# Kernel optimization log

Measured on AMD Instinct MI355X. Metric: run time of the kernel, lower is better.

Reference implementation:

```python
import jax, jax.numpy as jnp
import numpy as np

N_USERS = 200000
N_ITEMS = 100000
EMB_DIM = 64
N_LAYERS = 4
E_POS = 2000000
E_NEG = 500000


def _propagate(row, col, user_emb, item_emb, edge_weight, n_users, n_items):
    # LightGCN-style symmetric degree-normalized neighbor aggregation.
    deg_u = jnp.clip(jnp.zeros((n_users,), jnp.float32).at[row].add(1.0), 1.0)
    deg_i = jnp.clip(jnp.zeros((n_items,), jnp.float32).at[col].add(1.0), 1.0)
    norm = jax.lax.rsqrt(deg_u)[row] * jax.lax.rsqrt(deg_i)[col] * edge_weight  # [E]
    # gather -> scale -> scatter_add, both directions
    item_to_user = jnp.zeros_like(user_emb).at[row].add(item_emb[col] * norm[:, None])
    user_to_item = jnp.zeros_like(item_emb).at[col].add(user_emb[row] * norm[:, None])
    return user_emb + item_to_user, item_emb + user_to_item


def setup_inputs() -> dict:
    key = jax.random.key(0)
    k1, k2, k3, k4, k5, k6 = jax.random.split(key, 6)
    # Xavier-normal-ish init: std = sqrt(2/(fan_in+fan_out))
    std_u = np.sqrt(2.0 / (N_USERS + EMB_DIM)).astype(np.float32)
    std_i = np.sqrt(2.0 / (N_ITEMS + EMB_DIM)).astype(np.float32)
    return {
        "edge_index": jax.random.randint(k1, (2, E_POS), 0, N_ITEMS, dtype=jnp.int32),
        "negative_edge_index": jax.random.randint(k2, (2, E_NEG), 0, N_ITEMS, dtype=jnp.int32),
        "edge_weight": jnp.ones((E_POS,), jnp.float32),
        "user_emb_pos_w": jax.random.normal(k3, (N_USERS, EMB_DIM), jnp.float32) * std_u,
        "item_emb_pos_w": jax.random.normal(k4, (N_ITEMS, EMB_DIM), jnp.float32) * std_i,
        "user_emb_neg_w": jax.random.normal(k5, (N_USERS, EMB_DIM), jnp.float32) * std_u,
        "item_emb_neg_w": jax.random.normal(k6, (N_ITEMS, EMB_DIM), jnp.float32) * std_i,
    }


def reference(edge_index, negative_edge_index, edge_weight,
              user_emb_pos_w, item_emb_pos_w, user_emb_neg_w, item_emb_neg_w):
    row, col = edge_index[0], edge_index[1]
    nrow, ncol = negative_edge_index[0], negative_edge_index[1]
    neg_w = jnp.ones_like(nrow, dtype=jnp.float32)

    ue_p, ie_p = user_emb_pos_w, item_emb_pos_w
    ue_n, ie_n = user_emb_neg_w, item_emb_neg_w
    sum_up, sum_ip = ue_p, ie_p
    sum_un, sum_in = ue_n, ie_n
    for _ in range(N_LAYERS):
        ue_p, ie_p = _propagate(row, col, ue_p, ie_p, edge_weight, N_USERS, N_ITEMS)
        sum_up = sum_up + ue_p
        sum_ip = sum_ip + ie_p
    for _ in range(N_LAYERS):
        ue_n, ie_n = _propagate(nrow, ncol, ue_n, ie_n, neg_w, N_USERS, N_ITEMS)
        sum_un = sum_un + ue_n
        sum_in = sum_in + ie_n
    inv = 1.0 / (N_LAYERS + 1)
    return (sum_up * inv, sum_ip * inv, sum_un * inv, sum_in * inv)
```

## Files before the change

kernel.cpp:

```cpp
#include <hip/hip_runtime.h>

#define DIM 64
#define CHUNK 2048


__global__ void hist_kernel(const int* __restrict__ row, const int* __restrict__ col,
                            int* __restrict__ deg_u, int* __restrict__ deg_i, int E) {
    int e = blockIdx.x * blockDim.x + threadIdx.x;
    if (e < E) {
        atomicAdd(&deg_u[row[e]], 1);
        atomicAdd(&deg_i[col[e]], 1);
    }
}

__global__ void fill_rsqrt(const int* __restrict__ deg, float* __restrict__ r, int n) {
    int i = blockIdx.x * blockDim.x + threadIdx.x;
    if (i < n) r[i] = rsqrtf(fmaxf((float)deg[i], 1.0f));
}

__global__ void partial_sums(const int* __restrict__ deg, int* __restrict__ bsum, int n) {
    __shared__ int s[256];
    int t = threadIdx.x;
    int base = blockIdx.x * CHUNK + t * 8;
    int loc = 0;
    for (int k = 0; k < 8; k++) { int j = base + k; if (j < n) loc += deg[j]; }
    s[t] = loc; __syncthreads();
    for (int ofs = 128; ofs > 0; ofs >>= 1) { if (t < ofs) s[t] += s[t + ofs]; __syncthreads(); }
    if (t == 0) bsum[blockIdx.x] = s[0];
}

__global__ void scan_small(int* __restrict__ bsum, int nb) {
    if (threadIdx.x == 0 && blockIdx.x == 0) {
        int acc = 0;
        for (int i = 0; i < nb; i++) { int x = bsum[i]; bsum[i] = acc; acc += x; }
    }
}

__global__ void scan_chunk(const int* __restrict__ deg, int* __restrict__ offs,
                           int* __restrict__ cur, const int* __restrict__ bsum, int n) {
    __shared__ int s[256];
    int t = threadIdx.x;
    int base = blockIdx.x * CHUNK + t * 8;
    int v[8]; int loc = 0;
    for (int k = 0; k < 8; k++) { int j = base + k; v[k] = (j < n) ? deg[j] : 0; loc += v[k]; }
    s[t] = loc; __syncthreads();
    for (int ofs = 1; ofs < 256; ofs <<= 1) {
        int x = (t >= ofs) ? s[t - ofs] : 0;
        __syncthreads();
        s[t] += x;
        __syncthreads();
    }
    int excl = (t == 0) ? 0 : s[t - 1];
    int run = bsum[blockIdx.x] + excl;
    for (int k = 0; k < 8; k++) {
        int j = base + k;
        if (j < n) { offs[j] = run; cur[j] = run; }
        run += v[k];
    }
}

__global__ void scatter_kernel(const int* __restrict__ row, const int* __restrict__ col,
                               const float* __restrict__ w, int has_w,
                               const float* __restrict__ ru, const float* __restrict__ ri,
                               int* __restrict__ cur_u, int* __restrict__ cur_i,
                               int2* __restrict__ adj_u, int2* __restrict__ adj_i, int E) {
    int e = blockIdx.x * blockDim.x + threadIdx.x;
    if (e >= E) return;
    int r = row[e], c = col[e];
    float wv = has_w ? w[e] : 1.0f;
    float nrm = ru[r] * ri[c] * wv;
    int nb = __float_as_int(nrm);
    int pu = atomicAdd(&cur_u[r], 1);
    adj_u[pu] = make_int2(c, nb);
    int pi = atomicAdd(&cur_i[c], 1);
    adj_i[pi] = make_int2(r, nb);
}


__global__ void init2(const float* __restrict__ src, float* __restrict__ cur,
                      float* __restrict__ sum, int n4) {
    int i = blockIdx.x * blockDim.x + threadIdx.x;
    if (i < n4) {
        float4 v = ((const float4*)src)[i];
        ((float4*)cur)[i] = v;
        ((float4*)sum)[i] = v;
    }
}

__global__ void aggregate(const int* __restrict__ offs, const int* __restrict__ endo,
                          const int2* __restrict__ adj,
                          const float* __restrict__ src,
                          const float* __restrict__ self_old,
                          float* __restrict__ self_new,
                          float* __restrict__ sum,
                          float scale, int N) {
    int t = blockIdx.x * blockDim.x + threadIdx.x;
    int v = t >> 4;
    if (v >= N) return;
    int q = (t & 15) * 4;
    size_t rowoff = (size_t)v * DIM + q;
    float4 acc = *(const float4*)(self_old + rowoff);
    int s = offs[v], e = endo[v];
    int i = s;
    for (; i + 1 < e; i += 2) {
        int2 m0 = adj[i];
        int2 m1 = adj[i + 1];
        float n0 = __int_as_float(m0.y);
        float n1 = __int_as_float(m1.y);
        float4 b0 = *(const float4*)(src + (size_t)m0.x * DIM + q);
        float4 b1 = *(const float4*)(src + (size_t)m1.x * DIM + q);
        acc.x += b0.x * n0 + b1.x * n1;
        acc.y += b0.y * n0 + b1.y * n1;
        acc.z += b0.z * n0 + b1.z * n1;
        acc.w += b0.w * n0 + b1.w * n1;
    }
    if (i < e) {
        int2 m0 = adj[i];
        float n0 = __int_as_float(m0.y);
        float4 b0 = *(const float4*)(src + (size_t)m0.x * DIM + q);
        acc.x += b0.x * n0;
        acc.y += b0.y * n0;
        acc.z += b0.z * n0;
        acc.w += b0.w * n0;
    }
    *(float4*)(self_new + rowoff) = acc;
    float4 sm = *(const float4*)(sum + rowoff);
    sm.x = (sm.x + acc.x) * scale;
    sm.y = (sm.y + acc.y) * scale;
    sm.z = (sm.z + acc.z) * scale;
    sm.w = (sm.w + acc.w) * scale;
    *(float4*)(sum + rowoff) = sm;
}


static inline int cdiv(long long a, int b) { return (int)((a + b - 1) / b); }

extern "C" void kernel_launch(void* const* d_in, const int* in_sizes, int n_in,
                              void* d_out, int out_size, void* d_ws, size_t ws_size,
                              hipStream_t stream) {
    const int*   ei  = (const int*)d_in[0];
    const int*   nei = (const int*)d_in[1];
    const float* ew  = (const float*)d_in[2];
    const float* uep = (const float*)d_in[3];
    const float* iep = (const float*)d_in[4];
    const float* uen = (const float*)d_in[5];
    const float* ien = (const float*)d_in[6];
    float* out = (float*)d_out;

    const int E_POS = in_sizes[2];
    const int E_NEG = in_sizes[1] / 2;
    const int NU = in_sizes[3] / DIM;
    const int NI = in_sizes[4] / DIM;
    const int NTOT = (NU + NI) * DIM;

    char* ws = (char*)d_ws;
    size_t off = 0;
    auto alloc = [&](size_t elems4) { void* p = ws + off; off += elems4 * 4; return p; };
    float* u_emb  = (float*)alloc((size_t)NU * DIM);
    float* i_emb0 = (float*)alloc((size_t)NI * DIM);
    float* i_emb1 = (float*)alloc((size_t)NI * DIM);
    int*   offs_u = (int*)alloc(NU);
    int*   offs_i = (int*)alloc(NI);
    int*   cur_u  = (int*)alloc(NU);
    int*   cur_i  = (int*)alloc(NI);
    float* ru     = (float*)alloc(NU);
    float* ri     = (float*)alloc(NI);
    int*   bsum   = (int*)alloc(256);
    int2*  adj_u  = (int2*)alloc((size_t)E_POS * 2);
    int2*  adj_i  = (int2*)alloc((size_t)E_POS * 2);

    const int B = 256;
    const int nb_u = cdiv(NU, CHUNK);
    const int nb_i = cdiv(NI, CHUNK);

    for (int g = 0; g < 2; ++g) {
        const int    E   = g == 0 ? E_POS : E_NEG;
        const int*   row = g == 0 ? ei : nei;
        const int*   col = row + E;
        const float* wv  = g == 0 ? ew : nullptr;
        const float* ue0 = g == 0 ? uep : uen;
        const float* ie0 = g == 0 ? iep : ien;
        float* sum_u = out + (size_t)g * NTOT;
        float* sum_i = sum_u + (size_t)NU * DIM;

        hipMemsetAsync(cur_u, 0, (size_t)(NU + NI) * sizeof(int), stream);
        hist_kernel<<<cdiv(E, B), B, 0, stream>>>(row, col, cur_u, cur_i, E);
        fill_rsqrt<<<cdiv(NU, B), B, 0, stream>>>(cur_u, ru, NU);
        fill_rsqrt<<<cdiv(NI, B), B, 0, stream>>>(cur_i, ri, NI);
        partial_sums<<<nb_u, B, 0, stream>>>(cur_u, bsum, NU);
        scan_small<<<1, 64, 0, stream>>>(bsum, nb_u);
        scan_chunk<<<nb_u, B, 0, stream>>>(cur_u, offs_u, cur_u, bsum, NU);
        partial_sums<<<nb_i, B, 0, stream>>>(cur_i, bsum, NI);
        scan_small<<<1, 64, 0, stream>>>(bsum, nb_i);
        scan_chunk<<<nb_i, B, 0, stream>>>(cur_i, offs_i, cur_i, bsum, NI);
        scatter_kernel<<<cdiv(E, B), B, 0, stream>>>(row, col, wv, g == 0 ? 1 : 0,
                                                     ru, ri, cur_u, cur_i,
                                                     adj_u, adj_i, E);

        init2<<<cdiv(NU * DIM / 4, B), B, 0, stream>>>(ue0, u_emb, sum_u, NU * DIM / 4);
        init2<<<cdiv(NI * DIM / 4, B), B, 0, stream>>>(ie0, i_emb0, sum_i, NI * DIM / 4);

        float* icur = i_emb0;
        float* inew = i_emb1;
        for (int l = 0; l < 4; ++l) {
            float scale = (l == 3) ? 0.2f : 1.0f;
            aggregate<<<cdiv((long long)NI * 16, B), B, 0, stream>>>(
                offs_i, cur_i, adj_i, u_emb, icur, inew, sum_i, scale, NI);
            aggregate<<<cdiv((long long)NU * 16, B), B, 0, stream>>>(
                offs_u, cur_u, adj_u, icur, u_emb, u_emb, sum_u, scale, NU);
            float* t = icur; icur = inew; inew = t;
        }
    }
}
```

Baseline: 1.870 ms.

## Merge user/item CSR into one array and use wave-per-vertex aggregation

Builds a single combined degree/offset/adjacency structure for users and items, which halves the number of histogram-scan launches and replaces the serial single-thread block-sum scan with a parallel block scan. The aggregate kernel now assigns one 64-lane wavefront per vertex, with one float per lane, a wave-uniform vertex index and a 4-way unrolled neighbor loop, instead of 16 lanes per vertex using float4. This is meant to cut launch and serial-scan overhead and to raise memory-level parallelism in the gather. The tradeoff is narrower per-lane loads and more threads per vertex.

```diff
diff --git a/kernel.cpp b/kernel.cpp
--- a/kernel.cpp
+++ b/kernel.cpp
@@ -5,11 +5,11 @@
 
 
 __global__ void hist_kernel(const int* __restrict__ row, const int* __restrict__ col,
-                            int* __restrict__ deg_u, int* __restrict__ deg_i, int E) {
+                            int* __restrict__ deg, int NU, int E) {
     int e = blockIdx.x * blockDim.x + threadIdx.x;
     if (e < E) {
-        atomicAdd(&deg_u[row[e]], 1);
-        atomicAdd(&deg_i[col[e]], 1);
+        atomicAdd(&deg[row[e]], 1);
+        atomicAdd(&deg[NU + col[e]], 1);
     }
 }
 
@@ -29,11 +29,18 @@
     if (t == 0) bsum[blockIdx.x] = s[0];
 }
 
-__global__ void scan_small(int* __restrict__ bsum, int nb) {
-    if (threadIdx.x == 0 && blockIdx.x == 0) {
-        int acc = 0;
-        for (int i = 0; i < nb; i++) { int x = bsum[i]; bsum[i] = acc; acc += x; }
-    }
+__global__ void scan_block(int* __restrict__ bsum, int nb) {
+    __shared__ int s[256];
+    int t = threadIdx.x;
+    int x = (t < nb) ? bsum[t] : 0;
+    s[t] = x; __syncthreads();
+    for (int ofs = 1; ofs < 256; ofs <<= 1) {
+        int y = (t >= ofs) ? s[t - ofs] : 0;
+        __syncthreads();
+        s[t] += y;
+        __syncthreads();
+    }
+    if (t < nb) bsum[t] = s[t] - x;
 }
 
 __global__ void scan_chunk(const int* __restrict__ deg, int* __restrict__ offs,
@@ -61,19 +68,19 @@
 
 __global__ void scatter_kernel(const int* __restrict__ row, const int* __restrict__ col,
                                const float* __restrict__ w, int has_w,
-                               const float* __restrict__ ru, const float* __restrict__ ri,
-                               int* __restrict__ cur_u, int* __restrict__ cur_i,
-                               int2* __restrict__ adj_u, int2* __restrict__ adj_i, int E) {
+                               const float* __restrict__ rs,
+                               int* __restrict__ cur, int2* __restrict__ adj,
+                               int NU, int E) {
     int e = blockIdx.x * blockDim.x + threadIdx.x;
     if (e >= E) return;
     int r = row[e], c = col[e];
     float wv = has_w ? w[e] : 1.0f;
-    float nrm = ru[r] * ri[c] * wv;
+    float nrm = rs[r] * rs[NU + c] * wv;
     int nb = __float_as_int(nrm);
-    int pu = atomicAdd(&cur_u[r], 1);
-    adj_u[pu] = make_int2(c, nb);
-    int pi = atomicAdd(&cur_i[c], 1);
-    adj_i[pi] = make_int2(r, nb);
+    int pu = atomicAdd(&cur[r], 1);
+    adj[pu] = make_int2(c, nb);
+    int pi = atomicAdd(&cur[NU + c], 1);
+    adj[pi] = make_int2(r, nb);
 }
 
 
@@ -94,42 +101,35 @@
                           float* __restrict__ self_new,
                           float* __restrict__ sum,
                           float scale, int N) {
-    int t = blockIdx.x * blockDim.x + threadIdx.x;
-    int v = t >> 4;
+    int v = blockIdx.x * (blockDim.x >> 6) + (threadIdx.x >> 6);
     if (v >= N) return;
-    int q = (t & 15) * 4;
-    size_t rowoff = (size_t)v * DIM + q;
-    float4 acc = *(const float4*)(self_old + rowoff);
+    v = __builtin_amdgcn_readfirstlane(v);
+    int l = threadIdx.x & 63;
+    size_t rowoff = (size_t)v * DIM + l;
+    float acc = self_old[rowoff];
     int s = offs[v], e = endo[v];
     int i = s;
-    for (; i + 1 < e; i += 2) {
+    for (; i + 3 < e; i += 4) {
         int2 m0 = adj[i];
         int2 m1 = adj[i + 1];
-        float n0 = __int_as_float(m0.y);
-        float n1 = __int_as_float(m1.y);
-        float4 b0 = *(const float4*)(src + (size_t)m0.x * DIM + q);
-        float4 b1 = *(const float4*)(src + (size_t)m1.x * DIM + q);
-        acc.x += b0.x * n0 + b1.x * n1;
-        acc.y += b0.y * n0 + b1.y * n1;
-        acc.z += b0.z * n0 + b1.z * n1;
-        acc.w += b0.w * n0 + b1.w * n1;
-    }
-    if (i < e) {
-        int2 m0 = adj[i];
-        float n0 = __int_as_float(m0.y);
-        float4 b0 = *(const float4*)(src + (size_t)m0.x * DIM + q);
-        acc.x += b0.x * n0;
-        acc.y += b0.y * n0;
-        acc.z += b0.z * n0;
-        acc.w += b0.w * n0;
-    }
-    *(float4*)(self_new + rowoff) = acc;
-    float4 sm = *(const float4*)(sum + rowoff);
-    sm.x = (sm.x + acc.x) * scale;
-    sm.y = (sm.y + acc.y) * scale;
-    sm.z = (sm.z + acc.z) * scale;
-    sm.w = (sm.w + acc.w) * scale;
-    *(float4*)(sum + rowoff) = sm;
+        int2 m2 = adj[i + 2];
+        int2 m3 = adj[i + 3];
+        float b0 = src[(size_t)m0.x * DIM + l];
+        float b1 = src[(size_t)m1.x * DIM + l];
+        float b2 = src[(size_t)m2.x * DIM + l];
+        float b3 = src[(size_t)m3.x * DIM + l];
+        acc += b0 * __int_as_float(m0.y);
+        acc += b1 * __int_as_float(m1.y);
+        acc += b2 * __int_as_float(m2.y);
+        acc += b3 * __int_as_float(m3.y);
+    }
+    for (; i < e; i++) {
+        int2 m = adj[i];
+        acc += src[(size_t)m.x * DIM + l] * __int_as_float(m.y);
+    }
+    self_new[rowoff] = acc;
+    float sm = sum[rowoff];
+    sum[rowoff] = (sm + acc) * scale;
 }
 
 
@@ -151,27 +151,23 @@
     const int E_NEG = in_sizes[1] / 2;
     const int NU = in_sizes[3] / DIM;
     const int NI = in_sizes[4] / DIM;
-    const int NTOT = (NU + NI) * DIM;
+    const int NV = NU + NI;
+    const int NTOT = NV * DIM;
 
     char* ws = (char*)d_ws;
     size_t off = 0;
     auto alloc = [&](size_t elems4) { void* p = ws + off; off += elems4 * 4; return p; };
-    float* u_emb  = (float*)alloc((size_t)NU * DIM);
+    float* u_emb = (float*)alloc((size_t)NU * DIM);
     float* i_emb0 = (float*)alloc((size_t)NI * DIM);
     float* i_emb1 = (float*)alloc((size_t)NI * DIM);
-    int*   offs_u = (int*)alloc(NU);
-    int*   offs_i = (int*)alloc(NI);
-    int*   cur_u  = (int*)alloc(NU);
-    int*   cur_i  = (int*)alloc(NI);
-    float* ru     = (float*)alloc(NU);
-    float* ri     = (float*)alloc(NI);
-    int*   bsum   = (int*)alloc(256);
-    int2*  adj_u  = (int2*)alloc((size_t)E_POS * 2);
-    int2*  adj_i  = (int2*)alloc((size_t)E_POS * 2);
+    int*   offs = (int*)alloc(NV);
+    int*   cur  = (int*)alloc(NV);
+    float* rs   = (float*)alloc(NV);
+    int*   bsum = (int*)alloc(256);
+    int2*  adj  = (int2*)alloc((size_t)E_POS * 4);
 
     const int B = 256;
-    const int nb_u = cdiv(NU, CHUNK);
-    const int nb_i = cdiv(NI, CHUNK);
+    const int nb = cdiv(NV, CHUNK);
 
     for (int g = 0; g < 2; ++g) {
         const int    E   = g == 0 ? E_POS : E_NEG;
@@ -183,19 +179,14 @@
         float* sum_u = out + (size_t)g * NTOT;
         float* sum_i = sum_u + (size_t)NU * DIM;
 
-        hipMemsetAsync(cur_u, 0, (size_t)(NU + NI) * sizeof(int), stream);
-        hist_kernel<<<cdiv(E, B), B, 0, stream>>>(row, col, cur_u, cur_i, E);
-        fill_rsqrt<<<cdiv(NU, B), B, 0, stream>>>(cur_u, ru, NU);
-        fill_rsqrt<<<cdiv(NI, B), B, 0, stream>>>(cur_i, ri, NI);
-        partial_sums<<<nb_u, B, 0, stream>>>(cur_u, bsum, NU);
-        scan_small<<<1, 64, 0, stream>>>(bsum, nb_u);
-        scan_chunk<<<nb_u, B, 0, stream>>>(cur_u, offs_u, cur_u, bsum, NU);
-        partial_sums<<<nb_i, B, 0, stream>>>(cur_i, bsum, NI);
-        scan_small<<<1, 64, 0, stream>>>(bsum, nb_i);
-        scan_chunk<<<nb_i, B, 0, stream>>>(cur_i, offs_i, cur_i, bsum, NI);
+        hipMemsetAsync(cur, 0, (size_t)NV * sizeof(int), stream);
+        hist_kernel<<<cdiv(E, B), B, 0, stream>>>(row, col, cur, NU, E);
+        fill_rsqrt<<<cdiv(NV, B), B, 0, stream>>>(cur, rs, NV);
+        partial_sums<<<nb, B, 0, stream>>>(cur, bsum, NV);
+        scan_block<<<1, 256, 0, stream>>>(bsum, nb);
+        scan_chunk<<<nb, B, 0, stream>>>(cur, offs, cur, bsum, NV);
         scatter_kernel<<<cdiv(E, B), B, 0, stream>>>(row, col, wv, g == 0 ? 1 : 0,
-                                                     ru, ri, cur_u, cur_i,
-                                                     adj_u, adj_i, E);
+                                                     rs, cur, adj, NU, E);
 
         init2<<<cdiv(NU * DIM / 4, B), B, 0, stream>>>(ue0, u_emb, sum_u, NU * DIM / 4);
         init2<<<cdiv(NI * DIM / 4, B), B, 0, stream>>>(ie0, i_emb0, sum_i, NI * DIM / 4);
@@ -204,10 +195,10 @@
         float* inew = i_emb1;
         for (int l = 0; l < 4; ++l) {
             float scale = (l == 3) ? 0.2f : 1.0f;
-            aggregate<<<cdiv((long long)NI * 16, B), B, 0, stream>>>(
-                offs_i, cur_i, adj_i, u_emb, icur, inew, sum_i, scale, NI);
-            aggregate<<<cdiv((long long)NU * 16, B), B, 0, stream>>>(
-                offs_u, cur_u, adj_u, icur, u_emb, u_emb, sum_u, scale, NU);
+            aggregate<<<cdiv(NI, 4), B, 0, stream>>>(
+                offs + NU, cur + NU, adj, u_emb, icur, inew, sum_i, scale, NI);
+            aggregate<<<cdiv(NU, 4), B, 0, stream>>>(
+                offs, cur, adj, icur, u_emb, u_emb, sum_u, scale, NU);
             float* t = icur; icur = inew; inew = t;
         }
     }
```

Result: no change. 1.841 ms (-1.6%).
